# Kernel optimization log

Hardware: AMD Instinct MI355X
Metric: run time of the kernel (lower is better)

The kernel has to match this reference:

```python
import jax, jax.numpy as jnp
import numpy as np

EPS = 1e-16


def setup_inputs() -> dict:
    key = jax.random.key(0)
    k1, k2 = jax.random.split(key)
    p = jax.random.normal(k1, (2, 32, 2048, 4), dtype=jnp.float32)
    q = jax.random.normal(k2, (32, 2048, 4), dtype=jnp.float32)
    return {"p": p, "q": q}


def reference(p, q):
    # im=False path: take the real part of the complex generated momenta
    p_real = p[0]                      # (B, N, 4)
    # loss_norm_choice='p3', take_sqrt=True: use 3-momenta (drop energy)
    p3 = p_real[..., 1:]               # (B, N, 3)
    q3 = q[..., 1:]                    # (B, M, 3)
    # Pairwise Euclidean distance (cdist) via the expanded quadratic form to
    # avoid materializing the (B, N, M, 3) difference tensor.
    x2 = jnp.sum(p3 * p3, axis=-1)     # (B, N)
    y2 = jnp.sum(q3 * q3, axis=-1)     # (B, M)
    xy = jnp.einsum('bnd,bmd->bnm', p3, q3)  # (B, N, M)
    dist_sq = x2[..., :, None] + y2[..., None, :] - 2.0 * xy
    dist = jnp.sqrt(jnp.maximum(dist_sq, 0.0) + EPS)  # (B, N, M)
    # Bidirectional nearest-neighbor min-reduction
    min_pq = jnp.min(dist, axis=-1)    # (B, N)
    min_qp = jnp.min(dist, axis=-2)    # (B, M)
    chamfer_loss = jnp.sum((min_pq + min_qp) * 0.5)
    return chamfer_loss
```

## Files before the change

kernel.cpp:

```cpp
#include <hip/hip_runtime.h>
#include <math.h>


#define NPTS   2048
#define NBATCH 32
#define NSIDE  (NBATCH * NPTS)
#define SLAB32 (NSIDE * 2)
#define EPSF   1e-16f
#define BIGF   3.4e38f

typedef short bf16x8  __attribute__((ext_vector_type(8)));
typedef float f32x16  __attribute__((ext_vector_type(16)));

__device__ __forceinline__ short f2b(float f) {
    unsigned u = __float_as_uint(f);
    return (short)((u + 0x7FFFu + ((u >> 16) & 1u)) >> 16);
}
__device__ __forceinline__ float b2f(short h) {
    return __uint_as_float(((unsigned)(unsigned short)h) << 16);
}
__device__ __forceinline__ float min3f(float a, float b, float c) {
    return fminf(fminf(a, b), c);
}

__global__ __launch_bounds__(256) void chamfer_prep(
    const float* __restrict__ P, const float* __restrict__ Q,
    uint4* __restrict__ ws)
{
    const int i    = blockIdx.x * 256 + threadIdx.x;
    const int side = i >> 16;
    const int pt   = i & (NSIDE - 1);

    float4 v = ((const float4*)(side ? Q : P))[pt];
    const float cx = v.y, cy = v.z, cz = v.w;
    const short one = f2b(1.0f);

    float n2 = cx * cx + cy * cy + cz * cz;
    short n2h = f2b(n2); short n2l = f2b(n2 - b2f(n2h));
    float tx = -2.f * cx; short mhx = f2b(tx); short mlx = f2b(tx - b2f(mhx));
    float ty = -2.f * cy; short mhy = f2b(ty); short mly = f2b(ty - b2f(mhy));
    float tz = -2.f * cz; short mhz = f2b(tz); short mlz = f2b(tz - b2f(mhz));
    short qhx = f2b(cx), qlx = f2b(cx - b2f(qhx));
    short qhy = f2b(cy), qly = f2b(cy - b2f(qhy));
    short qhz = f2b(cz), qlz = f2b(cz - b2f(qhz));

    __align__(16) short a16[16] = { n2h, n2l, one, one,
                                    mhx, mhy, mhz, mhx, mhy, mhz,
                                    mlx, mly, mlz, mlx, mly, mlz };
    __align__(16) short b16[16] = { one, one, n2h, n2l,
                                    qhx, qhy, qhz, qlx, qly, qlz,
                                    qhx, qhy, qhz, qlx, qly, qlz };

    uint4* A = ws + (size_t)side * SLAB32 + (size_t)pt * 2;
    A[0] = ((const uint4*)a16)[0];
    A[1] = ((const uint4*)a16)[1];
    uint4* B = ws + (size_t)(side ? 2 : 3) * SLAB32 + (size_t)pt * 2;
    B[0] = ((const uint4*)b16)[0];
    B[1] = ((const uint4*)b16)[1];
}

__global__ __launch_bounds__(256) void chamfer_main(
    const uint4* __restrict__ ws, float* __restrict__ out)
{
    __shared__ float rbuf[4];
    const int tid  = threadIdx.x;
    const int w    = tid >> 6;
    const int lane = tid & 63;
    const int l31  = lane & 31;
    const int kh   = lane >> 5;

    const int bid  = blockIdx.x;
    const int b    = (bid & 7) + 8 * ((bid >> 3) & 3);
    const int rest = bid >> 5;
    const int dir  = rest & 1;
    const int bi   = rest >> 1;

    const uint4* Aslab = ws + (size_t)dir * SLAB32;
    const uint4* Bslab = ws + (size_t)(dir ? 3 : 2) * SLAB32;
    const size_t pbase = (size_t)b * NPTS;

    bf16x8 Af = *(const bf16x8*)&Aslab[(pbase + bi * 128 + w * 32 + l31) * 2 + kh];

    float rm[16];
    #pragma unroll
    for (int i = 0; i < 16; ++i) rm[i] = BIGF;

    const f32x16 z = {0.f,0.f,0.f,0.f, 0.f,0.f,0.f,0.f,
                      0.f,0.f,0.f,0.f, 0.f,0.f,0.f,0.f};

    const uint4* Bp = &Bslab[(pbase + l31) * 2 + kh];
    bf16x8 cur0 = *(const bf16x8*)(Bp);
    bf16x8 cur1 = *(const bf16x8*)(Bp + 64);
    #pragma unroll 4
    for (int g = 0; g < 31; ++g) {
        const uint4* nb = Bp + (size_t)(2 * g + 2) * 64;
        bf16x8 n0 = *(const bf16x8*)(nb);
        bf16x8 n1 = *(const bf16x8*)(nb + 64);
        f32x16 c0 = __builtin_amdgcn_mfma_f32_32x32x16_bf16(Af, cur0, z, 0, 0, 0);
        f32x16 c1 = __builtin_amdgcn_mfma_f32_32x32x16_bf16(Af, cur1, z, 0, 0, 0);
        #pragma unroll
        for (int i = 0; i < 16; ++i) rm[i] = min3f(rm[i], c0[i], c1[i]);
        cur0 = n0; cur1 = n1;
    }
    {
        f32x16 c0 = __builtin_amdgcn_mfma_f32_32x32x16_bf16(Af, cur0, z, 0, 0, 0);
        f32x16 c1 = __builtin_amdgcn_mfma_f32_32x32x16_bf16(Af, cur1, z, 0, 0, 0);
        #pragma unroll
        for (int i = 0; i < 16; ++i) rm[i] = min3f(rm[i], c0[i], c1[i]);
    }

    float s = 0.f;
    #pragma unroll
    for (int i = 0; i < 16; ++i) {
        float v = rm[i];
        v = fminf(v, __shfl_xor(v, 1));
        v = fminf(v, __shfl_xor(v, 2));
        v = fminf(v, __shfl_xor(v, 4));
        v = fminf(v, __shfl_xor(v, 8));
        v = fminf(v, __shfl_xor(v, 16));
        s += sqrtf(fmaxf(v, 0.f) + EPSF);
    }
    s += __shfl_xor(s, 32);

    if (lane == 0) rbuf[w] = s;
    __syncthreads();
    if (tid == 0)
        atomicAdd(out, 0.5f * ((rbuf[0] + rbuf[1]) + (rbuf[2] + rbuf[3])));
}

extern "C" void kernel_launch(void* const* d_in, const int* in_sizes, int n_in,
                              void* d_out, int out_size, void* d_ws, size_t ws_size,
                              hipStream_t stream) {
    const float* P = (const float*)d_in[0];
    const float* Q = (const float*)d_in[1];
    float* out = (float*)d_out;
    uint4* ws = (uint4*)d_ws;

    hipMemsetAsync(out, 0, sizeof(float), stream);

    chamfer_prep<<<dim3(512), 256, 0, stream>>>(P, Q, ws);

    chamfer_main<<<dim3(1024), 256, 0, stream>>>(ws, out);
}
```

Measured before the change: 87.40 us.

## Split column range across wave pairs and double grid size with LDS min-merge

Each block now handles 64 rows instead of 128. Two waves share each 32-row group, and each wave scans half of the 2048 columns. Partial row minima are merged through shared memory before the sqrt and the atomic add. The grid doubles to 2048 blocks, which shortens each wave's serial loop and raises the number of blocks available to fill the GPU. The B-operand prefetch is also deepened to two iterations ahead, using wraparound indexing that issues a few redundant loads. The cost is an extra barrier, more A-fragment loads overall, and twice as many atomics.

```diff
diff --git a/kernel.cpp b/kernel.cpp
--- a/kernel.cpp
+++ b/kernel.cpp
@@ -62,15 +62,17 @@
 __global__ __launch_bounds__(256) void chamfer_main(
     const uint4* __restrict__ ws, float* __restrict__ out)
 {
-    __shared__ float rbuf[4];
+    __shared__ float srow[4][32];
     const int tid  = threadIdx.x;
     const int w    = tid >> 6;
     const int lane = tid & 63;
     const int l31  = lane & 31;
     const int kh   = lane >> 5;
+    const int rg   = w >> 1;
+    const int ch   = w & 1;
 
     const int bid  = blockIdx.x;
-    const int b    = (bid & 7) + 8 * ((bid >> 3) & 3);
+    const int b    = (bid & 7) | (((bid >> 3) & 3) << 3);
     const int rest = bid >> 5;
     const int dir  = rest & 1;
     const int bi   = rest >> 1;
@@ -79,7 +81,7 @@
     const uint4* Bslab = ws + (size_t)(dir ? 3 : 2) * SLAB32;
     const size_t pbase = (size_t)b * NPTS;
 
-    bf16x8 Af = *(const bf16x8*)&Aslab[(pbase + bi * 128 + w * 32 + l31) * 2 + kh];
+    bf16x8 Af = *(const bf16x8*)&Aslab[(pbase + bi * 64 + rg * 32 + l31) * 2 + kh];
 
     float rm[16];
     #pragma unroll
@@ -88,28 +90,23 @@
     const f32x16 z = {0.f,0.f,0.f,0.f, 0.f,0.f,0.f,0.f,
                       0.f,0.f,0.f,0.f, 0.f,0.f,0.f,0.f};
 
-    const uint4* Bp = &Bslab[(pbase + l31) * 2 + kh];
-    bf16x8 cur0 = *(const bf16x8*)(Bp);
-    bf16x8 cur1 = *(const bf16x8*)(Bp + 64);
+    const uint4* Bp = &Bslab[(pbase + ch * 1024 + l31) * 2 + kh];
+    bf16x8 b0 = *(const bf16x8*)(Bp);
+    bf16x8 b1 = *(const bf16x8*)(Bp + 64);
+    bf16x8 b2 = *(const bf16x8*)(Bp + 128);
+    bf16x8 b3 = *(const bf16x8*)(Bp + 192);
     #pragma unroll 4
-    for (int g = 0; g < 31; ++g) {
-        const uint4* nb = Bp + (size_t)(2 * g + 2) * 64;
-        bf16x8 n0 = *(const bf16x8*)(nb);
-        bf16x8 n1 = *(const bf16x8*)(nb + 64);
-        f32x16 c0 = __builtin_amdgcn_mfma_f32_32x32x16_bf16(Af, cur0, z, 0, 0, 0);
-        f32x16 c1 = __builtin_amdgcn_mfma_f32_32x32x16_bf16(Af, cur1, z, 0, 0, 0);
+    for (int t = 0; t < 32; t += 2) {
+        const int tn = (t + 4) & 31;
+        bf16x8 n0 = *(const bf16x8*)(Bp + tn * 64);
+        bf16x8 n1 = *(const bf16x8*)(Bp + tn * 64 + 64);
+        f32x16 c0 = __builtin_amdgcn_mfma_f32_32x32x16_bf16(Af, b0, z, 0, 0, 0);
+        f32x16 c1 = __builtin_amdgcn_mfma_f32_32x32x16_bf16(Af, b1, z, 0, 0, 0);
         #pragma unroll
         for (int i = 0; i < 16; ++i) rm[i] = min3f(rm[i], c0[i], c1[i]);
-        cur0 = n0; cur1 = n1;
-    }
-    {
-        f32x16 c0 = __builtin_amdgcn_mfma_f32_32x32x16_bf16(Af, cur0, z, 0, 0, 0);
-        f32x16 c1 = __builtin_amdgcn_mfma_f32_32x32x16_bf16(Af, cur1, z, 0, 0, 0);
-        #pragma unroll
-        for (int i = 0; i < 16; ++i) rm[i] = min3f(rm[i], c0[i], c1[i]);
+        b0 = b2; b1 = b3; b2 = n0; b3 = n1;
     }
 
-    float s = 0.f;
     #pragma unroll
     for (int i = 0; i < 16; ++i) {
         float v = rm[i];
@@ -118,14 +115,19 @@
         v = fminf(v, __shfl_xor(v, 4));
         v = fminf(v, __shfl_xor(v, 8));
         v = fminf(v, __shfl_xor(v, 16));
-        s += sqrtf(fmaxf(v, 0.f) + EPSF);
+        if (l31 == 0)
+            srow[w][(i & 3) + 8 * (i >> 2) + 4 * kh] = v;
     }
-    s += __shfl_xor(s, 32);
+    __syncthreads();
 
-    if (lane == 0) rbuf[w] = s;
-    __syncthreads();
-    if (tid == 0)
-        atomicAdd(out, 0.5f * ((rbuf[0] + rbuf[1]) + (rbuf[2] + rbuf[3])));
+    if (tid < 64) {
+        const int g = tid >> 5, r = tid & 31;
+        float v = fminf(srow[2 * g][r], srow[2 * g + 1][r]);
+        float s = sqrtf(fmaxf(v, 0.f) + EPSF);
+        #pragma unroll
+        for (int off = 32; off > 0; off >>= 1) s += __shfl_down(s, off);
+        if (tid == 0) atomicAdd(out, 0.5f * s);
+    }
 }
 
 extern "C" void kernel_launch(void* const* d_in, const int* in_sizes, int n_in,
@@ -140,5 +142,5 @@
 
     chamfer_prep<<<dim3(512), 256, 0, stream>>>(P, Q, ws);
 
-    chamfer_main<<<dim3(1024), 256, 0, stream>>>(ws, out);
+    chamfer_main<<<dim3(2048), 256, 0, stream>>>(ws, out);
 }
```

Result: slower. 99.85 us (+14.2%).
